# Kernel optimization log

Measured on AMD Instinct MI355X. Metric: run time of the kernel, lower is better.

Reference implementation:

```python
import jax, jax.numpy as jnp
from jax import lax
import numpy as np

B, T, C_IN, H, W = 2, 4, 128, 64, 64
D_MODEL, N_Q, N_POINTS, PATCH, N_LAYERS = 256, 300, 8, 3, 6


def _sine_pos(Hh, Ww, d, temperature=10000.0):
    # mask is all-False, so cumsum of ones -> arange(1..H)/H * 2pi
    two_pi = 2.0 * np.pi
    yn = (jnp.arange(1, Hh + 1, dtype=jnp.float32) / (Hh + 1e-6)) * two_pi
    xn = (jnp.arange(1, Ww + 1, dtype=jnp.float32) / (Ww + 1e-6)) * two_pi
    q = d // 4
    i = jnp.arange(q, dtype=jnp.float32)
    dim_t = temperature ** (2.0 * jnp.floor(i / 2.0) / q)
    py = yn[:, None] / dim_t
    px = xn[:, None] / dim_t
    py = jnp.stack([jnp.sin(py), jnp.cos(py)], axis=-1).reshape(Hh, 2 * q)
    px = jnp.stack([jnp.sin(px), jnp.cos(px)], axis=-1).reshape(Ww, 2 * q)
    pos = jnp.concatenate([
        jnp.broadcast_to(py[:, None, :], (Hh, Ww, 2 * q)),
        jnp.broadcast_to(px[None, :, :], (Hh, Ww, 2 * q)),
    ], axis=-1)
    return jnp.transpose(pos, (2, 0, 1))  # [d,H,W]


def _sample_scale(fmap, ref, ps):
    # fmap [B,C,h,w]; ref [B,nQ,nP,2] in [0,1]. Bilinear grid_sample,
    # padding_mode='border', align_corners=True -> direct gather (no replication).
    Bc, C, h, w = fmap.shape
    half = (ps - 1) / 2.0
    off = jnp.linspace(-half, half, ps, dtype=jnp.float32)
    oy, ox = jnp.meshgrid(off, off, indexing='ij')  # [ps,ps]
    gx = ref[..., 0, None, None] * 2.0 - 1.0 + ox * (2.0 / w)  # [B,nQ,nP,ps,ps]
    gy = ref[..., 1, None, None] * 2.0 - 1.0 + oy * (2.0 / h)
    x = jnp.clip((gx + 1.0) * 0.5 * (w - 1), 0.0, w - 1.0)
    y = jnp.clip((gy + 1.0) * 0.5 * (h - 1), 0.0, h - 1.0)
    x0 = jnp.floor(x); y0 = jnp.floor(y)
    wx = x - x0; wy = y - y0
    x0i = x0.astype(jnp.int32); y0i = y0.astype(jnp.int32)
    x1i = jnp.minimum(x0i + 1, w - 1); y1i = jnp.minimum(y0i + 1, h - 1)

    def per_b(fb, y0b, x0b, y1b, x1b, wxb, wyb):
        v00 = fb[:, y0b, x0b]  # [C,nQ,nP,ps,ps]
        v01 = fb[:, y0b, x1b]
        v10 = fb[:, y1b, x0b]
        v11 = fb[:, y1b, x1b]
        return (v00 * (1 - wxb) * (1 - wyb) + v01 * wxb * (1 - wyb)
                + v10 * (1 - wxb) * wyb + v11 * wxb * wyb)

    out = jax.vmap(per_b)(fmap, y0i, x0i, y1i, x1i, wx, wy)  # [B,C,nQ,nP,ps,ps]
    return jnp.transpose(out, (0, 2, 3, 4, 5, 1))  # [B,nQ,nP,ps,ps,C]


def reference(feat, pred_boxes_init, w_tf, b_tf, w_in, b_in, w_lat, b_lat, w_sm, b_sm,
              q_embed, q_pos, Wq, bq, Wo, bo, Wp1, bp1, Wp2, bp2,
              w_r1, b_r1, w_r2, b_r2, w_b1, b_b1, w_b2, b_b2, w_cls, b_cls):
    Bb, Tt, Cin, Hh, Ww = feat.shape
    d = w_in.shape[0]
    nP = w_r2.shape[0] // 2
    ps = int(round((Wp1.shape[-1] // d) ** 0.5))
    # temporal fuse: Conv3d kernel (3,1,1), padding (1,0,0)
    x = lax.conv_general_dilated(jnp.transpose(feat, (0, 2, 1, 3, 4)), w_tf,
                                 (1, 1, 1), [(1, 1), (0, 0), (0, 0)],
                                 dimension_numbers=('NCDHW', 'OIDHW', 'NCDHW'))
    x = x + b_tf[None, :, None, None, None]
    x = x.mean(axis=2)  # [B,Cin,H,W]
    x = jnp.einsum('bchw,dc->bdhw', x, w_in) + b_in[None, :, None, None]
    x = x + _sine_pos(Hh, Ww, d)[None]
    # FPN over scales {1,2,4}: avg_pool -> 1x1 lateral -> 3x3 smooth
    feats = []
    for i, s in enumerate((1, 2, 4)):
        xi = x if s == 1 else x.reshape(Bb, d, Hh // s, s, Ww // s, s).mean(axis=(3, 5))
        xi = jnp.einsum('bchw,oc->bohw', xi, w_lat[i]) + b_lat[i][None, :, None, None]
        xi = lax.conv_general_dilated(xi, w_sm[i], (1, 1), [(1, 1), (1, 1)],
                                      dimension_numbers=('NCHW', 'OIHW', 'NCHW'))
        xi = xi + b_sm[i][None, :, None, None]
        feats.append(xi)
    nQ = q_embed.shape[0]
    queries = jnp.broadcast_to((q_embed + q_pos)[None], (Bb, nQ, d))
    boxes = pred_boxes_init
    inv_sqrt_d = 1.0 / float(np.sqrt(d))
    for l in range(Wq.shape[0]):
        h1 = jax.nn.relu(jnp.einsum('bqd,od->bqo', queries, w_r1) + b_r1)
        ro = jnp.tanh(jnp.einsum('bqd,od->bqo', h1, w_r2) + b_r2)
        ro = ro.reshape(Bb, nQ, nP, 2) * 0.5
        ref = jnp.clip(boxes[:, :, None, :2] + ro, 0.0, 1.0)
        sampled = jnp.concatenate([_sample_scale(f, ref, ps) for f in feats], axis=2)
        sampled = sampled[:, :, :nP]  # truncate multi-scale concat back to nP
        flat = sampled.reshape(Bb, nQ, nP, ps * ps * d)
        pv = jax.nn.relu(jnp.einsum('bqpi,oi->bqpo', flat, Wp1[l]) + bp1[l])
        pv = jnp.einsum('bqpd,od->bqpo', pv, Wp2[l]) + bp2[l]
        kv = pv.mean(axis=2)  # [B,nP_q,d] -> [B,nQ,d]
        q = jnp.einsum('bqd,od->bqo', queries, Wq[l]) + bq[l]
        attn = jax.nn.softmax(jnp.einsum('bqd,bkd->bqk', q, kv) * inv_sqrt_d, axis=-1)
        out = jnp.einsum('bqk,bkd->bqd', attn, kv)
        queries = queries + (jnp.einsum('bqd,od->bqo', out, Wo[l]) + bo[l])
        hb = jax.nn.relu(jnp.einsum('bqd,od->bqo', queries, w_b1) + b_b1)
        delta = jax.nn.sigmoid(jnp.einsum('bqd,od->bqo', hb, w_b2) + b_b2)
        boxes = jnp.clip(boxes + 0.1 * jnp.tanh(delta - 0.5), 0.0, 1.0)
    logits = (jnp.einsum('bqd,od->bqo', queries, w_cls) + b_cls)[..., 0]
    return logits, boxes


def setup_inputs() -> dict:
    key = jax.random.key(0)
    keys = iter(jax.random.split(key, 48))

    def nrm(shape, s=0.02):
        return jax.random.normal(next(keys), shape, dtype=jnp.float32) * s

    inp = {
        'feat': jax.random.normal(next(keys), (B, T, C_IN, H, W), dtype=jnp.float32),
        'pred_boxes_init': jax.random.uniform(next(keys), (B, N_Q, 4), dtype=jnp.float32),
        'w_tf': nrm((C_IN, C_IN, 3, 1, 1)), 'b_tf': jnp.zeros((C_IN,), jnp.float32),
        'w_in': nrm((D_MODEL, C_IN)), 'b_in': jnp.zeros((D_MODEL,), jnp.float32),
        'w_lat': nrm((3, D_MODEL, D_MODEL)), 'b_lat': jnp.zeros((3, D_MODEL), jnp.float32),
        'w_sm': nrm((3, D_MODEL, D_MODEL, 3, 3)), 'b_sm': jnp.zeros((3, D_MODEL), jnp.float32),
        'q_embed': nrm((N_Q, D_MODEL), 1.0), 'q_pos': nrm((N_Q, D_MODEL), 1.0),
        'Wq': nrm((N_LAYERS, D_MODEL, D_MODEL)), 'bq': jnp.zeros((N_LAYERS, D_MODEL), jnp.float32),
        'Wo': nrm((N_LAYERS, D_MODEL, D_MODEL)), 'bo': jnp.zeros((N_LAYERS, D_MODEL), jnp.float32),
        'Wp1': nrm((N_LAYERS, D_MODEL, PATCH * PATCH * D_MODEL)), 'bp1': jnp.zeros((N_LAYERS, D_MODEL), jnp.float32),
        'Wp2': nrm((N_LAYERS, D_MODEL, D_MODEL)), 'bp2': jnp.zeros((N_LAYERS, D_MODEL), jnp.float32),
        'w_r1': nrm((D_MODEL, D_MODEL)), 'b_r1': jnp.zeros((D_MODEL,), jnp.float32),
        'w_r2': nrm((2 * N_POINTS, D_MODEL)), 'b_r2': jnp.zeros((2 * N_POINTS,), jnp.float32),
        'w_b1': nrm((D_MODEL, D_MODEL)), 'b_b1': jnp.zeros((D_MODEL,), jnp.float32),
        'w_b2': nrm((4, D_MODEL)), 'b_b2': jnp.zeros((4,), jnp.float32),
        'w_cls': nrm((1, D_MODEL)), 'b_cls': jnp.zeros((1,), jnp.float32),
    }
    return inp
```

## Files before the change

### kernel.cpp

```cpp
#include <hip/hip_runtime.h>
#include <hip/hip_bf16.h>
#include <math.h>

#define BB 2
#define TT 4
#define CIN 128
#define DM 256
#define NQ 300
#define NP 8
#define PS 3
#define NL 6
#define HW 4096
#define KP 2304

typedef __attribute__((ext_vector_type(8))) short short8;
typedef __attribute__((ext_vector_type(4))) short short4_t;
typedef __attribute__((ext_vector_type(4))) float f32x4;
typedef unsigned short ushort_t;

static __device__ __forceinline__ ushort_t f2bf(float f) {
  __hip_bfloat16 h = __float2bfloat16(f);
  return *reinterpret_cast<ushort_t*>(&h);
}
static __device__ __forceinline__ float bf2f(ushort_t u) {
  return __uint_as_float(((unsigned)u) << 16);
}

__global__ void k_prep(const float* __restrict__ w_in, const float* __restrict__ w_lat,
                       const float* __restrict__ w_b1,
                       const float* __restrict__ w_r1, const float* __restrict__ Wp1,
                       ushort_t* __restrict__ win_bf, ushort_t* __restrict__ wlat_bf,
                       ushort_t* __restrict__ wb1_bf,
                       ushort_t* __restrict__ wr1_bf, ushort_t* __restrict__ wp1_bf,
                       const float* __restrict__ w_tf, ushort_t* __restrict__ tct,
                       const float* __restrict__ w_sm, ushort_t* __restrict__ wsm_bf,
                       const float* __restrict__ Wp2, const float* __restrict__ Wo,
                       const float* __restrict__ bq, const float* __restrict__ bp2,
                       const float* __restrict__ bo,
                       float* __restrict__ bqt, float* __restrict__ bfuse,
                       uint4* __restrict__ x2p_zero,
                       const float* __restrict__ b_tf, const float* __restrict__ b_in,
                       float* __restrict__ bias_comb,
                       const float* __restrict__ qe, const float* __restrict__ qp,
                       const float* __restrict__ pb, float* __restrict__ queries,
                       ushort_t* __restrict__ qbf, float* __restrict__ boxes,
                       const float* __restrict__ feat, ushort_t* __restrict__ featT) {
  __shared__ float ldsF[64][65];
  float* bt = &ldsF[0][0];
  int b = blockIdx.x, t = threadIdx.x;
  if (b < 3680) {
    int i = b * 256 + t;
    const float* s; ushort_t* d; int base;
    if (i < 8192)         { s = w_in;  d = win_bf;  base = 0; }
    else if (i < 24576)   { s = w_lat; d = wlat_bf; base = 8192; }
    else if (i < 40960)   { s = w_b1;  d = wb1_bf;  base = 24576; }
    else if (i < 57344)   { s = w_r1;  d = wr1_bf;  base = 40960; }
    else                  { s = Wp1;   d = wp1_bf;  base = 57344; }
    int j = i - base;
    float4 v = ((const float4*)s)[j];
    d[j * 4 + 0] = f2bf(v.x);
    d[j * 4 + 1] = f2bf(v.y);
    d[j * 4 + 2] = f2bf(v.z);
    d[j * 4 + 3] = f2bf(v.w);
  } else if (b < 3936) {
    int i = (b - 3680) * 256 + t;
    int k = i >> 7, c = i & 127;
    int u = k >> 7, ci = k & 127;
    const float* wp = w_tf + ((size_t)(c * 128 + ci)) * 3;
    float w0 = wp[0], w1 = wp[1], w2 = wp[2];
    float coef = (u == 0) ? (w0 + w1) : (u == 3) ? (w1 + w2) : (w0 + w1 + w2);
    tct[(size_t)k * 128 + c] = f2bf(0.25f * coef);
  } else if (b < 6240) {
    int i = (b - 3936) * 256 + t;
    int n = i / KP;
    int r = i - n * KP;
    int tp = r >> 8, c = r & 255;
    wsm_bf[i] = f2bf(w_sm[((size_t)(n * 256 + c)) * 9 + tp]);
  } else if (b < 6252) {
    int i = (b - 6240) * 256 + t;
    if (i < 1536) {
      int l = i >> 8, d = i & 255;
      float a = 0.f;
      for (int o = 0; o < 256; ++o)
        a += bq[l * 256 + o] * Wp2[((size_t)(l * 256 + o)) * 256 + d];
      bqt[i] = a;
    } else {
      int j = i - 1536;
      int l = j >> 8, o2 = j & 255;
      float a = bo[l * 256 + o2];
      for (int o = 0; o < 256; ++o)
        a += bp2[l * 256 + o] * Wo[((size_t)(l * 256 + o2)) * 256 + o];
      bfuse[j] = a;
    }
  } else if (b < 7341) {
    int j = (b - 6252) * 256 + t;
    if (j < 278784) x2p_zero[j] = make_uint4(0u, 0u, 0u, 0u);
  } else if (b < 7342) {
    int d = t;
    if (d < 128) bt[d] = b_tf[d];
    __syncthreads();
    float a = b_in[d];
    for (int c = 0; c < 128; ++c) a += w_in[d * 128 + c] * bt[c];
    bias_comb[d] = a;
  } else if (b < 7942) {
    int i = (b - 7342) * 256 + t;
    if (i < BB * NQ * DM) {
      int rd = i % (NQ * DM);
      float v = qe[rd] + qp[rd];
      queries[i] = v;
      qbf[i] = f2bf(v);
    }
    if (i < BB * NQ * 4) boxes[i] = pb[i];
  } else {
    int idx = b - 7942;
    int gs = idx & 127;
    int k0 = (idx >> 7) * 64;
    int bb = gs >> 6;
    int s0 = (gs & 63) * 64;
    int kk = t >> 2, sc0 = (t & 3) * 16;
    {
      int k = k0 + kk;
      int u = k >> 7, ci = k & 127;
      const float* src = feat + (((size_t)(bb * 4 + u) * 128 + ci) << 12) + s0 + sc0;
#pragma unroll
      for (int j = 0; j < 4; ++j) {
        float4 v = *(const float4*)(src + j * 4);
        ldsF[kk][sc0 + j * 4 + 0] = v.x;
        ldsF[kk][sc0 + j * 4 + 1] = v.y;
        ldsF[kk][sc0 + j * 4 + 2] = v.z;
        ldsF[kk][sc0 + j * 4 + 3] = v.w;
      }
    }
    __syncthreads();
#pragma unroll
    for (int p = 0; p < 2; ++p) {
      int idx2 = p * 256 + t;
      int s_l = idx2 >> 3, kc = (idx2 & 7) * 8;
      short8 v;
#pragma unroll
      for (int j = 0; j < 8; ++j) v[j] = (short)f2bf(ldsF[kc + j][s_l]);
      *(short8*)(featT + (size_t)(bb * 4096 + s0 + s_l) * 512 + k0 + kc) = v;
    }
  }
}

__global__ __launch_bounds__(256) void k_wcompose(const float* __restrict__ Wp2,
                                                  const float* __restrict__ Wq,
                                                  const float* __restrict__ Wo,
                                                  ushort_t* __restrict__ wqt,
                                                  ushort_t* __restrict__ wfuseT) {
  __shared__ ushort_t As[64 * 36];
  __shared__ ushort_t Bs[64 * 36];
  int z = blockIdx.z, l = z % 6;
  const float* Asrc = Wp2 + (size_t)l * 65536;
  const float* Bsrc = ((z < 6) ? Wq : Wo) + (size_t)l * 65536;
  ushort_t* C = ((z < 6) ? wqt : wfuseT) + (size_t)l * 65536;
  bool btr = (z < 6);
  int tid = threadIdx.x;
  int bm = blockIdx.x * 64, bn = blockIdx.y * 64;
  int w = tid >> 6, lane = tid & 63;
  int wm = (w & 1) * 32, wn = (w >> 1) * 32;
  int q = lane >> 4, ml = lane & 15;
  f32x4 acc[2][2] = {};
  int oo = tid >> 3, mg = (tid & 7) * 8;
  int nr = tid >> 2, kg = (tid & 3) * 8;
  for (int k0 = 0; k0 < 256; k0 += 32) {
    {
      const float* sp = Asrc + (size_t)(k0 + oo) * 256 + bm + mg;
      float4 f0 = *(const float4*)sp;
      float4 f1 = *(const float4*)(sp + 4);
      ushort_t* dst = As + oo;
      dst[(mg + 0) * 36] = f2bf(f0.x); dst[(mg + 1) * 36] = f2bf(f0.y);
      dst[(mg + 2) * 36] = f2bf(f0.z); dst[(mg + 3) * 36] = f2bf(f0.w);
      dst[(mg + 4) * 36] = f2bf(f1.x); dst[(mg + 5) * 36] = f2bf(f1.y);
      dst[(mg + 6) * 36] = f2bf(f1.z); dst[(mg + 7) * 36] = f2bf(f1.w);
    }
    if (btr) {
      const float* sp = Bsrc + (size_t)(k0 + oo) * 256 + bn + mg;
      float4 f0 = *(const float4*)sp;
      float4 f1 = *(const float4*)(sp + 4);
      ushort_t* dst = Bs + oo;
      dst[(mg + 0) * 36] = f2bf(f0.x); dst[(mg + 1) * 36] = f2bf(f0.y);
      dst[(mg + 2) * 36] = f2bf(f0.z); dst[(mg + 3) * 36] = f2bf(f0.w);
      dst[(mg + 4) * 36] = f2bf(f1.x); dst[(mg + 5) * 36] = f2bf(f1.y);
      dst[(mg + 6) * 36] = f2bf(f1.z); dst[(mg + 7) * 36] = f2bf(f1.w);
    } else {
      const float* sp = Bsrc + (size_t)(bn + nr) * 256 + k0 + kg;
      float4 f0 = *(const float4*)sp;
      float4 f1 = *(const float4*)(sp + 4);
      short8 v;
      v[0] = (short)f2bf(f0.x); v[1] = (short)f2bf(f0.y);
      v[2] = (short)f2bf(f0.z); v[3] = (short)f2bf(f0.w);
      v[4] = (short)f2bf(f1.x); v[5] = (short)f2bf(f1.y);
      v[6] = (short)f2bf(f1.z); v[7] = (short)f2bf(f1.w);
      *(short8*)(Bs + nr * 36 + kg) = v;
    }
    __syncthreads();
    short8 a0 = *(const short8*)(As + (wm + ml) * 36 + q * 8);
    short8 a1 = *(const short8*)(As + (wm + 16 + ml) * 36 + q * 8);
    short8 b0 = *(const short8*)(Bs + (wn + ml) * 36 + q * 8);
    short8 b1 = *(const short8*)(Bs + (wn + 16 + ml) * 36 + q * 8);
    acc[0][0] = __builtin_amdgcn_mfma_f32_16x16x32_bf16(a0, b0, acc[0][0], 0, 0, 0);
    acc[0][1] = __builtin_amdgcn_mfma_f32_16x16x32_bf16(a0, b1, acc[0][1], 0, 0, 0);
    acc[1][0] = __builtin_amdgcn_mfma_f32_16x16x32_bf16(a1, b0, acc[1][0], 0, 0, 0);
    acc[1][1] = __builtin_amdgcn_mfma_f32_16x16x32_bf16(a1, b1, acc[1][1], 0, 0, 0);
    __syncthreads();
  }
#pragma unroll
  for (int i = 0; i < 2; ++i)
#pragma unroll
    for (int j = 0; j < 2; ++j) {
      int cn = bn + wn + j * 16 + ml;
#pragma unroll
      for (int r = 0; r < 4; ++r) {
        int rm = bm + wm + i * 16 + q * 4 + r;
        C[(size_t)rm * 256 + cn] = f2bf(acc[i][j][r]);
      }
    }
}

__global__ __launch_bounds__(256) void k_feat2(const ushort_t* __restrict__ featT,
                                               const ushort_t* __restrict__ wcomb,
                                               const float* __restrict__ biasc,
                                               ushort_t* __restrict__ xcl) {
  __shared__ ushort_t As[32 * 72];
  __shared__ ushort_t Bs[64 * 72];
  __shared__ float dimt_s[256];
  int tid = threadIdx.x;
  {
    int dd = tid & 127;
    int ii = dd >> 1;
    dimt_s[tid] = powf(10000.0f, (2.0f * (float)(ii >> 1)) / 64.0f);
  }
  int bm = blockIdx.x * 32, bn = blockIdx.y * 64;
  int w = tid >> 6, lane = tid & 63;
  int wm = (w & 1) * 16, wn = (w >> 1) * 32;
  int q = lane >> 4, ml = lane & 15;
  int sra = tid >> 3, sca = (tid & 7) * 8;
  int srb = tid >> 2, scb = (tid & 3) * 16;
  const ushort_t* Ag = featT + (size_t)(bm + sra) * 512 + sca;
  const ushort_t* Wg = wcomb + (size_t)(bn + srb) * 512 + scb;
  f32x4 acc[2] = {};
  short8 av = *(const short8*)Ag;
  short8 wv0 = *(const short8*)Wg;
  short8 wv1 = *(const short8*)(Wg + 8);
  for (int k0 = 0; k0 < 512; k0 += 64) {
    *(short8*)(As + sra * 72 + sca) = av;
    *(short8*)(Bs + srb * 72 + scb) = wv0;
    *(short8*)(Bs + srb * 72 + scb + 8) = wv1;
    __syncthreads();
    if (k0 + 64 < 512) {
      av = *(const short8*)(Ag + k0 + 64);
      wv0 = *(const short8*)(Wg + k0 + 64);
      wv1 = *(const short8*)(Wg + k0 + 72);
    }
#pragma unroll
    for (int h = 0; h < 2; ++h) {
      int kc = h * 32 + q * 8;
      short8 a = *(const short8*)(As + (wm + ml) * 72 + kc);
      short8 b0 = *(const short8*)(Bs + (wn + ml) * 72 + kc);
      short8 b1 = *(const short8*)(Bs + (wn + 16 + ml) * 72 + kc);
      acc[0] = __builtin_amdgcn_mfma_f32_16x16x32_bf16(a, b0, acc[0], 0, 0, 0);
      acc[1] = __builtin_amdgcn_mfma_f32_16x16x32_bf16(a, b1, acc[1], 0, 0, 0);
    }
    __syncthreads();
  }
  const float FKT = 6.28318530717958647692f / 64.000001f;
#pragma unroll
  for (int j = 0; j < 2; ++j) {
    int cn = bn + wn + j * 16 + ml;
    float dimt = dimt_s[cn];
    float bC = biasc[cn];
    bool isx = cn >= 128;
    bool isc = cn & 1;
#pragma unroll
    for (int r = 0; r < 4; ++r) {
      int rm = bm + wm + q * 4 + r;
      int s = rm & 4095;
      int y = s >> 6, x = s & 63;
      float ang = (float)((isx ? x : y) + 1) * FKT / dimt;
      float pos = isc ? cosf(ang) : sinf(ang);
      xcl[(size_t)rm * 256 + cn] = f2bf(acc[j][r] + bC + pos);
    }
  }
}

template <int ACT, int OUTMODE, int MG>
__global__ __launch_bounds__(256) void k_gemm_bf16(const ushort_t* __restrict__ A,
                                                   const ushort_t* __restrict__ W,
                                                   const float* __restrict__ bias,
                                                   const float* __restrict__ res,
                                                   float* __restrict__ Cf,
                                                   ushort_t* __restrict__ Cb,
                                                   int M, int N, int K,
                                                   const ushort_t* __restrict__ W2,
                                                   const float* __restrict__ bias2,
                                                   const ushort_t* __restrict__ W3,
                                                   const float* __restrict__ bias3) {
  __shared__ ushort_t As[64 * 72];
  __shared__ ushort_t Bs[64 * 72];
  int tid = threadIdx.x;
  int bm = blockIdx.x * 64, bn = blockIdx.y * 64;
  int w = tid >> 6, lane = tid & 63;
  int wm = (w & 1) * 32, wn = (w >> 1) * 32;
  int q = lane >> 4, ml = lane & 15;
  f32x4 acc[2][2] = {};
  int srow = tid >> 2, scol = (tid & 3) * 16;
  int ga = bm + srow;
  if (MG) ga = min(ga, M - 1);
  const ushort_t* Ag = A + (size_t)ga * K + scol;
  const ushort_t* Wg;
  if (OUTMODE == 7) {
    int seg = bn >> 8;
    const ushort_t* Wb = (seg == 0) ? W : ((seg == 1) ? W2 : W3);
    Wg = Wb + (size_t)((bn & 255) + srow) * K + scol;
  } else if (OUTMODE == 4) {
    const ushort_t* Wb = (bn < 256) ? W : W2;
    Wg = Wb + (size_t)((bn & 255) + srow) * K + scol;
  } else {
    Wg = W + (size_t)(bn + srow) * K + scol;
  }
  short8 av0 = *(const short8*)(Ag);
  short8 av1 = *(const short8*)(Ag + 8);
  short8 wv0 = *(const short8*)(Wg);
  short8 wv1 = *(const short8*)(Wg + 8);
  for (int k0 = 0; k0 < K; k0 += 64) {
    *(short8*)(As + srow * 72 + scol) = av0;
    *(short8*)(As + srow * 72 + scol + 8) = av1;
    *(short8*)(Bs + srow * 72 + scol) = wv0;
    *(short8*)(Bs + srow * 72 + scol + 8) = wv1;
    __syncthreads();
    if (k0 + 64 < K) {
      av0 = *(const short8*)(Ag + k0 + 64);
      av1 = *(const short8*)(Ag + k0 + 72);
      wv0 = *(const short8*)(Wg + k0 + 64);
      wv1 = *(const short8*)(Wg + k0 + 72);
    }
#pragma unroll
    for (int h = 0; h < 2; ++h) {
      int kc = h * 32 + q * 8;
      short8 a0 = *(const short8*)(As + (wm + ml) * 72 + kc);
      short8 a1 = *(const short8*)(As + (wm + 16 + ml) * 72 + kc);
      short8 b0 = *(const short8*)(Bs + (wn + ml) * 72 + kc);
      short8 b1 = *(const short8*)(Bs + (wn + 16 + ml) * 72 + kc);
      acc[0][0] = __builtin_amdgcn_mfma_f32_16x16x32_bf16(a0, b0, acc[0][0], 0, 0, 0);
      acc[0][1] = __builtin_amdgcn_mfma_f32_16x16x32_bf16(a0, b1, acc[0][1], 0, 0, 0);
      acc[1][0] = __builtin_amdgcn_mfma_f32_16x16x32_bf16(a1, b0, acc[1][0], 0, 0, 0);
      acc[1][1] = __builtin_amdgcn_mfma_f32_16x16x32_bf16(a1, b1, acc[1][1], 0, 0, 0);
    }
    __syncthreads();
  }
#pragma unroll
  for (int i = 0; i < 2; ++i) {
#pragma unroll
    for (int j = 0; j < 2; ++j) {
      int cn = bn + wn + j * 16 + ml;
      float bsv;
      if (OUTMODE == 7) {
        int seg = cn >> 8;
        bsv = ((seg == 0) ? bias : ((seg == 1) ? bias2 : bias3))[cn & 255];
      } else if (OUTMODE == 4) {
        bsv = ((cn < 256) ? bias : bias2)[cn & 255];
      } else {
        bsv = bias ? bias[cn] : 0.f;
      }
#pragma unroll
      for (int r = 0; r < 4; ++r) {
        int rm = bm + wm + i * 16 + q * 4 + r;
        if (MG && rm >= M) continue;
        float v = acc[i][j][r] + bsv;
        if (OUTMODE == 0) {
          if (ACT == 1) v = fmaxf(v, 0.f);
          Cf[(size_t)rm * N + cn] = v;
        } else if (OUTMODE == 1) {
          int b = rm >> 12, rem = rm & 4095;
          int y = rem >> 6, xx = rem & 63;
          Cb[(((size_t)(b * 66 + y + 1)) * 66 + xx + 1) * 256 + cn] = f2bf(v);
        } else if (OUTMODE == 4) {
          if (cn < 256) Cf[(size_t)rm * 256 + cn] = fmaxf(v, 0.f);
          else Cb[(size_t)rm * 256 + (cn & 255)] = f2bf(v);
        } else if (OUTMODE == 6) {
          Cb[(size_t)rm * N + cn] = f2bf(v);
        } else if (OUTMODE == 7) {
          if (cn < 256) Cf[(size_t)rm * 256 + cn] = fmaxf(v, 0.f);
          else if (cn < 512) ((float*)Cb)[(size_t)rm * 256 + (cn & 255)] = fmaxf(v, 0.f);
          else ((ushort_t*)res)[(size_t)rm * 256 + (cn & 255)] = f2bf(v);
        }
      }
    }
  }
}

__global__ __launch_bounds__(256) void k_wp1_split(const ushort_t* __restrict__ A,
                                                   const ushort_t* __restrict__ W,
                                                   ushort_t* __restrict__ part) {
  __shared__ ushort_t As[64 * 72];
  __shared__ ushort_t Bs[64 * 72];
  int tid = threadIdx.x;
  int bm = blockIdx.x * 64, bn = blockIdx.y * 64;
  int kz = blockIdx.z * 768;
  int w = tid >> 6, lane = tid & 63;
  int wm = (w & 1) * 32, wn = (w >> 1) * 32;
  int q = lane >> 4, ml = lane & 15;
  int srow = tid >> 2, scol = (tid & 3) * 16;
  const ushort_t* Ag = A + (size_t)(bm + srow) * KP + kz + scol;
  const ushort_t* Wg = W + (size_t)(bn + srow) * KP + kz + scol;
  f32x4 acc[2][2] = {};
  short8 av0 = *(const short8*)(Ag);
  short8 av1 = *(const short8*)(Ag + 8);
  short8 wv0 = *(const short8*)(Wg);
  short8 wv1 = *(const short8*)(Wg + 8);
  for (int k0 = 0; k0 < 768; k0 += 64) {
    *(short8*)(As + srow * 72 + scol) = av0;
    *(short8*)(As + srow * 72 + scol + 8) = av1;
    *(short8*)(Bs + srow * 72 + scol) = wv0;
    *(short8*)(Bs + srow * 72 + scol + 8) = wv1;
    __syncthreads();
    if (k0 + 64 < 768) {
      av0 = *(const short8*)(Ag + k0 + 64);
      av1 = *(const short8*)(Ag + k0 + 72);
      wv0 = *(const short8*)(Wg + k0 + 64);
      wv1 = *(const short8*)(Wg + k0 + 72);
    }
#pragma unroll
    for (int h = 0; h < 2; ++h) {
      int kc = h * 32 + q * 8;
      short8 a0 = *(const short8*)(As + (wm + ml) * 72 + kc);
      short8 a1 = *(const short8*)(As + (wm + 16 + ml) * 72 + kc);
      short8 b0 = *(const short8*)(Bs + (wn + ml) * 72 + kc);
      short8 b1 = *(const short8*)(Bs + (wn + 16 + ml) * 72 + kc);
      acc[0][0] = __builtin_amdgcn_mfma_f32_16x16x32_bf16(a0, b0, acc[0][0], 0, 0, 0);
      acc[0][1] = __builtin_amdgcn_mfma_f32_16x16x32_bf16(a0, b1, acc[0][1], 0, 0, 0);
      acc[1][0] = __builtin_amdgcn_mfma_f32_16x16x32_bf16(a1, b0, acc[1][0], 0, 0, 0);
      acc[1][1] = __builtin_amdgcn_mfma_f32_16x16x32_bf16(a1, b1, acc[1][1], 0, 0, 0);
    }
    __syncthreads();
  }
  ushort_t* pz = part + (size_t)blockIdx.z * 4800 * 256;
#pragma unroll
  for (int i = 0; i < 2; ++i)
#pragma unroll
    for (int j = 0; j < 2; ++j) {
      int cn = bn + wn + j * 16 + ml;
#pragma unroll
      for (int r = 0; r < 4; ++r) {
        int rm = bm + wm + i * 16 + q * 4 + r;
        pz[(size_t)rm * 256 + cn] = f2bf(acc[i][j][r]);
      }
    }
}

__global__ __launch_bounds__(256) void k_wp1_reduce(const ushort_t* __restrict__ part,
                                                    const float* __restrict__ bias,
                                                    ushort_t* __restrict__ pvm) {
  int row = blockIdx.x;
  int d = threadIdx.x;
  float b = bias[d];
  float s = 0.f;
#pragma unroll
  for (int p = 0; p < 8; ++p) {
    size_t idx = (size_t)(row * 8 + p) * 256 + d;
    float v = bf2f(part[idx]) + bf2f(part[idx + (size_t)4800 * 256]) +
              bf2f(part[idx + (size_t)2 * 4800 * 256]) + b;
    s += fmaxf(v, 0.f);
  }
  pvm[(size_t)row * 256 + d] = f2bf(s * 0.125f);
}

__global__ __launch_bounds__(256) void k_conv3(const ushort_t* __restrict__ x2p,
                                               const ushort_t* __restrict__ wsm,
                                               const float* __restrict__ bsm,
                                               ushort_t* __restrict__ fcl) {
  __shared__ ushort_t As[32 * 72];
  __shared__ ushort_t Bs[64 * 72];
  int tid = threadIdx.x;
  int bm = blockIdx.x * 32, bn = blockIdx.y * 64;
  int w = tid >> 6, lane = tid & 63;
  int wm = (w & 1) * 16, wn = (w >> 1) * 32;
  int q = lane >> 4, ml = lane & 15;
  int sra = tid >> 3, sca = (tid & 7) * 8;
  int srb = tid >> 2, scb = (tid & 3) * 16;
  int sA = bm + sra;
  int b = sA >> 12, rem = sA & 4095;
  size_t pbase = ((size_t)(b * 66 + (rem >> 6)) * 66 + (rem & 63)) * 256;
  const ushort_t* Wg = wsm + (size_t)(bn + srb) * KP + scb;
  auto loadA = [&](int k0) {
    int ka = k0 + sca;
    int t9 = ka >> 8;
    int ky = t9 / 3, kx = t9 - ky * 3;
    return *(const short8*)(x2p + pbase + (size_t)(ky * 66 + kx) * 256 + (ka & 255));
  };
  f32x4 acc[2] = {};
  short8 av = loadA(0);
  short8 wv0 = *(const short8*)(Wg);
  short8 wv1 = *(const short8*)(Wg + 8);
  for (int k0 = 0; k0 < KP; k0 += 64) {
    *(short8*)(As + sra * 72 + sca) = av;
    *(short8*)(Bs + srb * 72 + scb) = wv0;
    *(short8*)(Bs + srb * 72 + scb + 8) = wv1;
    __syncthreads();
    if (k0 + 64 < KP) {
      av = loadA(k0 + 64);
      wv0 = *(const short8*)(Wg + k0 + 64);
      wv1 = *(const short8*)(Wg + k0 + 72);
    }
#pragma unroll
    for (int h = 0; h < 2; ++h) {
      int kc = h * 32 + q * 8;
      short8 a = *(const short8*)(As + (wm + ml) * 72 + kc);
      short8 b0 = *(const short8*)(Bs + (wn + ml) * 72 + kc);
      short8 b1 = *(const short8*)(Bs + (wn + 16 + ml) * 72 + kc);
      acc[0] = __builtin_amdgcn_mfma_f32_16x16x32_bf16(a, b0, acc[0], 0, 0, 0);
      acc[1] = __builtin_amdgcn_mfma_f32_16x16x32_bf16(a, b1, acc[1], 0, 0, 0);
    }
    __syncthreads();
  }
#pragma unroll
  for (int j = 0; j < 2; ++j) {
    int cn = bn + wn + j * 16 + ml;
    float bsv = bsm[cn];
#pragma unroll
    for (int r = 0; r < 4; ++r) {
      int rm = bm + wm + q * 4 + r;
      fcl[(size_t)rm * 256 + cn] = f2bf(acc[j][r] + bsv);
    }
  }
}

__global__ __launch_bounds__(256) void k_sample(const ushort_t* __restrict__ fcl,
                                                const float* __restrict__ h1,
                                                const float* __restrict__ w_r2,
                                                const float* __restrict__ b_r2,
                                                const float* __restrict__ boxesIn,
                                                float* __restrict__ boxesOut,
                                                const float* __restrict__ hb,
                                                const float* __restrict__ w_b2,
                                                const float* __restrict__ b_b2,
                                                ushort_t* __restrict__ flat) {
  __shared__ float pr[8];
  __shared__ float bc2[2];
  __shared__ float nb2[2];
  int blk = blockIdx.x;
  int row = blk >> 3, p = blk & 7;
  int b = row / NQ;
  int tid = threadIdx.x;
  int w = tid >> 6, lane = tid & 63;
  if (hb) {
    float4 hv = *(const float4*)(hb + (size_t)row * 256 + lane * 4);
    float4 wv = *(const float4*)(w_b2 + (size_t)w * 256 + lane * 4);
    float aa = hv.x * wv.x + hv.y * wv.y + hv.z * wv.z + hv.w * wv.w;
#pragma unroll
    for (int s = 32; s > 0; s >>= 1) aa += __shfl_down(aa, s, 64);
    if (lane == 0) {
      aa += b_b2[w];
      float delta = 1.0f / (1.0f + expf(-aa));
      float v = boxesIn[row * 4 + w] + 0.1f * tanhf(delta - 0.5f);
      v = fminf(fmaxf(v, 0.f), 1.f);
      if (w < 2) nb2[w] = v;
      if (p == 0) boxesOut[row * 4 + w] = v;
    }
  } else if (tid < 2) {
    nb2[tid] = boxesIn[row * 4 + tid];
  }
  float h = h1[(size_t)row * 256 + tid];
  float px = h * w_r2[(size_t)(2 * p) * 256 + tid];
  float py = h * w_r2[(size_t)(2 * p + 1) * 256 + tid];
#pragma unroll
  for (int s = 32; s > 0; s >>= 1) {
    px += __shfl_down(px, s, 64);
    py += __shfl_down(py, s, 64);
  }
  if (lane == 0) { pr[w * 2] = px; pr[w * 2 + 1] = py; }
  __syncthreads();
  if (tid == 0) {
    float sx = pr[0] + pr[2] + pr[4] + pr[6] + b_r2[2 * p];
    float sy = pr[1] + pr[3] + pr[5] + pr[7] + b_r2[2 * p + 1];
    float rx = nb2[0] + 0.5f * tanhf(sx);
    float ry = nb2[1] + 0.5f * tanhf(sy);
    bc2[0] = fminf(fmaxf(rx, 0.f), 1.f);
    bc2[1] = fminf(fmaxf(ry, 0.f), 1.f);
  }
  __syncthreads();
  float rx = bc2[0], ry = bc2[1];
  const ushort_t* fb = fcl + (size_t)b * HW * DM;
  ushort_t* op = flat + (size_t)blk * KP;
  int c4 = (tid & 63) * 4;
  int g = tid >> 6;
  int p0 = (g == 0) ? 0 : (1 + 2 * g);
  int p1 = (g == 0) ? 3 : (3 + 2 * g);
  for (int p9 = p0; p9 < p1; ++p9) {
    int jy = (p9 >= 6) ? 2 : ((p9 >= 3) ? 1 : 0);
    int jx = p9 - jy * 3;
    float yy = (ry + (float)(jy - 1) * (1.0f / 64.0f)) * 63.0f;
    yy = fminf(fmaxf(yy, 0.f), 63.0f);
    float y0f = floorf(yy);
    float wy = yy - y0f;
    int y0 = (int)y0f;
    int y1 = min(y0 + 1, 63);
    float xx = (rx + (float)(jx - 1) * (1.0f / 64.0f)) * 63.0f;
    xx = fminf(fmaxf(xx, 0.f), 63.0f);
    float x0f = floorf(xx);
    float wx = xx - x0f;
    int x0 = (int)x0f;
    int x1 = min(x0 + 1, 63);
    short4_t v00 = *(const short4_t*)(fb + (y0 * 64 + x0) * DM + c4);
    short4_t v01 = *(const short4_t*)(fb + (y0 * 64 + x1) * DM + c4);
    short4_t v10 = *(const short4_t*)(fb + (y1 * 64 + x0) * DM + c4);
    short4_t v11 = *(const short4_t*)(fb + (y1 * 64 + x1) * DM + c4);
    short4_t ov;
#pragma unroll
    for (int jj = 0; jj < 4; ++jj) {
      float v = bf2f((ushort_t)v00[jj]) * (1.f - wx) * (1.f - wy) +
                bf2f((ushort_t)v01[jj]) * wx * (1.f - wy) +
                bf2f((ushort_t)v10[jj]) * (1.f - wx) * wy +
                bf2f((ushort_t)v11[jj]) * wx * wy;
      ov[jj] = (short)f2bf(v);
    }
    *(short4_t*)(op + p9 * DM + c4) = ov;
  }
}

__global__ __launch_bounds__(256) void k_attn(const ushort_t* __restrict__ qt,
                                              const ushort_t* __restrict__ pvm,
                                              const ushort_t* __restrict__ wfT,
                                              const float* __restrict__ bfuse_l,
                                              float* __restrict__ queries,
                                              ushort_t* __restrict__ qbf) {
  __shared__ float qs[256];
  __shared__ float sc[512];
  __shared__ float red[256];
  __shared__ float pr4[1024];
  int row = blockIdx.x;
  int b = row / NQ;
  int tid = threadIdx.x;
  qs[tid] = bf2f(qt[(size_t)row * DM + tid]);
  __syncthreads();
  const ushort_t* kvB = pvm + (size_t)b * NQ * DM;
#pragma unroll
  for (int s2 = 0; s2 < 2; ++s2) {
    int k = tid + s2 * 256;
    float v = -1e30f;
    if (k < NQ) {
      const ushort_t* kp = kvB + (size_t)k * DM;
      float a = 0.f;
#pragma unroll
      for (int d = 0; d < 256; d += 8) {
        short8 k8 = *(const short8*)(kp + d);
        const float* qd = qs + d;
        a += bf2f((ushort_t)k8[0]) * qd[0];
        a += bf2f((ushort_t)k8[1]) * qd[1];
        a += bf2f((ushort_t)k8[2]) * qd[2];
        a += bf2f((ushort_t)k8[3]) * qd[3];
        a += bf2f((ushort_t)k8[4]) * qd[4];
        a += bf2f((ushort_t)k8[5]) * qd[5];
        a += bf2f((ushort_t)k8[6]) * qd[6];
        a += bf2f((ushort_t)k8[7]) * qd[7];
      }
      v = a * (1.0f / 16.0f);
    }
    sc[k] = v;
  }
  __syncthreads();
  red[tid] = fmaxf(sc[tid], sc[tid + 256]);
  __syncthreads();
  for (int st = 128; st > 0; st >>= 1) {
    if (tid < st) red[tid] = fmaxf(red[tid], red[tid + st]);
    __syncthreads();
  }
  float mx = red[0];
  __syncthreads();
  float e0 = (tid < NQ) ? expf(sc[tid] - mx) : 0.f;
  float e1 = (tid + 256 < NQ) ? expf(sc[tid + 256] - mx) : 0.f;
  sc[tid] = e0;
  sc[tid + 256] = e1;
  red[tid] = e0 + e1;
  __syncthreads();
  for (int st = 128; st > 0; st >>= 1) {
    if (tid < st) red[tid] += red[tid + st];
    __syncthreads();
  }
  float inv = 1.0f / red[0];
  __syncthreads();
  float acc = 0.f;
#pragma unroll 4
  for (int k = 0; k < NQ; ++k)
    acc += sc[k] * bf2f(kvB[(size_t)k * DM + tid]);
  qs[tid] = acc * inv;
  __syncthreads();
  int oq = (tid & 63) * 4, dq = (tid >> 6) * 64;
  float a0 = 0.f, a1 = 0.f, a2 = 0.f, a3 = 0.f;
  const ushort_t* wp = wfT + (size_t)dq * 256 + oq;
#pragma unroll 8
  for (int dd = 0; dd < 64; ++dd) {
    float cc = qs[dq + dd];
    short4_t wv = *(const short4_t*)(wp + (size_t)dd * 256);
    a0 += cc * bf2f((ushort_t)wv[0]);
    a1 += cc * bf2f((ushort_t)wv[1]);
    a2 += cc * bf2f((ushort_t)wv[2]);
    a3 += cc * bf2f((ushort_t)wv[3]);
  }
  float* pb4 = pr4 + (tid >> 6) * 256 + oq;
  pb4[0] = a0; pb4[1] = a1; pb4[2] = a2; pb4[3] = a3;
  __syncthreads();
  float v = pr4[tid] + pr4[256 + tid] + pr4[512 + tid] + pr4[768 + tid] +
            bfuse_l[tid] + queries[(size_t)row * DM + tid];
  queries[(size_t)row * DM + tid] = v;
  qbf[(size_t)row * DM + tid] = f2bf(v);
}

__global__ __launch_bounds__(256) void k_boxf(const float* __restrict__ hb,
                                              const float* __restrict__ w_b2,
                                              const float* __restrict__ b_b2,
                                              float* __restrict__ boxes,
                                              int last,
                                              const float* __restrict__ queries,
                                              const float* __restrict__ w_cls,
                                              const float* __restrict__ b_cls,
                                              float* __restrict__ out) {
  __shared__ float nb[4];
  int row = blockIdx.x;
  int tid = threadIdx.x;
  int j = tid >> 6, lane = tid & 63;
  float4 hv = *(const float4*)(hb + (size_t)row * 256 + lane * 4);
  float4 wv = *(const float4*)(w_b2 + (size_t)j * 256 + lane * 4);
  float aa = hv.x * wv.x + hv.y * wv.y + hv.z * wv.z + hv.w * wv.w;
#pragma unroll
  for (int s = 32; s > 0; s >>= 1) aa += __shfl_down(aa, s, 64);
  if (lane == 0) {
    aa += b_b2[j];
    float delta = 1.0f / (1.0f + expf(-aa));
    float v = boxes[row * 4 + j] + 0.1f * tanhf(delta - 0.5f);
    v = fminf(fmaxf(v, 0.f), 1.f);
    boxes[row * 4 + j] = v;
    nb[j] = v;
  }
  if (last) {
    __syncthreads();
    if (j == 0) {
      float4 qv = *(const float4*)(queries + (size_t)row * 256 + lane * 4);
      float4 cv = *(const float4*)(w_cls + lane * 4);
      float a2 = qv.x * cv.x + qv.y * cv.y + qv.z * cv.z + qv.w * cv.w;
#pragma unroll
      for (int s = 32; s > 0; s >>= 1) a2 += __shfl_down(a2, s, 64);
      if (lane == 0) out[row] = a2 + b_cls[0];
    } else if (j == 1 && lane < 4) {
      out[600 + row * 4 + lane] = nb[lane];
    }
  }
}

extern "C" void kernel_launch(void* const* d_in, const int* in_sizes, int n_in,
                              void* d_out, int out_size, void* d_ws, size_t ws_size,
                              hipStream_t stream) {
  const float* feat   = (const float*)d_in[0];
  const float* pb     = (const float*)d_in[1];
  const float* w_tf   = (const float*)d_in[2];
  const float* b_tf   = (const float*)d_in[3];
  const float* w_in   = (const float*)d_in[4];
  const float* b_in   = (const float*)d_in[5];
  const float* w_lat  = (const float*)d_in[6];
  const float* b_lat  = (const float*)d_in[7];
  const float* w_sm   = (const float*)d_in[8];
  const float* b_sm   = (const float*)d_in[9];
  const float* q_embed= (const float*)d_in[10];
  const float* q_pos  = (const float*)d_in[11];
  const float* Wq     = (const float*)d_in[12];
  const float* bq     = (const float*)d_in[13];
  const float* Wo     = (const float*)d_in[14];
  const float* bo     = (const float*)d_in[15];
  const float* Wp1    = (const float*)d_in[16];
  const float* bp1    = (const float*)d_in[17];
  const float* Wp2    = (const float*)d_in[18];
  const float* bp2    = (const float*)d_in[19];
  const float* w_r1   = (const float*)d_in[20];
  const float* b_r1   = (const float*)d_in[21];
  const float* w_r2   = (const float*)d_in[22];
  const float* b_r2   = (const float*)d_in[23];
  const float* w_b1   = (const float*)d_in[24];
  const float* b_b1   = (const float*)d_in[25];
  const float* w_b2   = (const float*)d_in[26];
  const float* b_b2   = (const float*)d_in[27];
  const float* w_cls  = (const float*)d_in[28];
  const float* b_cls  = (const float*)d_in[29];
  float* out = (float*)d_out;

  float* ws = (float*)d_ws;
  size_t off = 0;
  auto alloc = [&](size_t n) { float* p = ws + off; off += n; return p; };
  ushort_t* flat    = (ushort_t*)alloc(5529600);
  ushort_t* part    = (ushort_t*)alloc(1843200);
  ushort_t* featT   = (ushort_t*)alloc(2097152);
  ushort_t* xcl     = (ushort_t*)alloc(1048576);
  ushort_t* x2p     = (ushort_t*)alloc(1115136);
  ushort_t* fcl     = (ushort_t*)alloc(1048576);
  ushort_t* wcomb   = (ushort_t*)alloc(65536);
  ushort_t* tct     = (ushort_t*)alloc(32768);
  ushort_t* win_bf  = (ushort_t*)alloc(16384);
  float*    biasc   = alloc(256);
  ushort_t* wlat_bf = (ushort_t*)alloc(32768);
  ushort_t* wsm_bf  = (ushort_t*)alloc(294912);
  ushort_t* wp1_bf  = (ushort_t*)alloc(1769472);
  ushort_t* wb1_bf  = (ushort_t*)alloc(32768);
  ushort_t* wr1_bf  = (ushort_t*)alloc(32768);
  ushort_t* wqt_bf  = (ushort_t*)alloc(196608);
  ushort_t* wfuseT  = (ushort_t*)alloc(196608);
  float*    bqt     = alloc(1536);
  float*    bfuse   = alloc(1536);
  float* queries = alloc(153600);
  ushort_t* qbf  = (ushort_t*)alloc(76800);
  float* h1      = alloc(153600);
  ushort_t* qt   = (ushort_t*)alloc(76800);
  float* hb      = alloc(153600);
  ushort_t* pvm  = (ushort_t*)alloc(76800);
  float* boxesA  = alloc(2400);
  float* boxesB  = alloc(2400);
  (void)ws_size; (void)in_sizes; (void)n_in; (void)out_size;

  k_prep<<<8966, 256, 0, stream>>>(w_in, w_lat, w_b1, w_r1, Wp1,
                                   win_bf, wlat_bf, wb1_bf, wr1_bf, wp1_bf,
                                   w_tf, tct, w_sm, wsm_bf,
                                   Wp2, Wo, bq, bp2, bo, bqt, bfuse,
                                   (uint4*)x2p, b_tf, b_in, biasc,
                                   q_embed, q_pos, pb, queries, qbf, boxesA,
                                   feat, featT);
  k_gemm_bf16<0, 6, 0><<<dim3(4, 8), 256, 0, stream>>>(win_bf, tct, nullptr, nullptr,
                                                       nullptr, wcomb, 256, 512, 128,
                                                       nullptr, nullptr, nullptr, nullptr);
  k_wcompose<<<dim3(4, 4, 12), 256, 0, stream>>>(Wp2, Wq, Wo, wqt_bf, wfuseT);

  k_feat2<<<dim3(256, 4), 256, 0, stream>>>(featT, wcomb, biasc, xcl);
  k_gemm_bf16<0, 1, 0><<<dim3(128, 4), 256, 0, stream>>>(xcl, wlat_bf, b_lat, nullptr,
                                                         nullptr, x2p, BB * HW, 256, 256,
                                                         nullptr, nullptr, nullptr, nullptr);
  k_conv3<<<dim3(256, 4), 256, 0, stream>>>(x2p, wsm_bf, b_sm, fcl);

  const int M6 = BB * NQ;
  const int Mp = BB * NQ * NP;
  dim3 g600w((M6 + 63) / 64, 8);
  dim3 g600m((M6 + 63) / 64, 12);
  dim3 gsk(Mp / 64, 4, 3);

  k_gemm_bf16<0, 4, 1><<<g600w, 256, 0, stream>>>(qbf, wr1_bf, b_r1, nullptr, h1,
                                                  qt, M6, 512, 256,
                                                  wqt_bf, bqt, nullptr, nullptr);
  float* bcur = boxesA;
  float* bnext = boxesB;
  for (int l = 0; l < NL; ++l) {
    const float* hbp = (l == 0) ? nullptr : hb;
    k_sample<<<Mp, 256, 0, stream>>>(fcl, h1, w_r2, b_r2, bcur, bnext,
                                     hbp, w_b2, b_b2, flat);
    if (l > 0) { float* tmp = bcur; bcur = bnext; bnext = tmp; }
    k_wp1_split<<<gsk, 256, 0, stream>>>(flat, wp1_bf + (size_t)l * 256 * KP, part);
    k_wp1_reduce<<<600, 256, 0, stream>>>(part, bp1 + (size_t)l * DM, pvm);
    k_attn<<<M6, 256, 0, stream>>>(qt, pvm, wfuseT + (size_t)l * 65536,
                                   bfuse + l * 256, queries, qbf);
    int ln = (l + 1) % NL;
    k_gemm_bf16<0, 7, 1><<<g600m, 256, 0, stream>>>(qbf, wb1_bf, b_b1, (const float*)qt,
                                                    hb, (ushort_t*)h1, M6, 768, 256,
                                                    wr1_bf, b_r1,
                                                    wqt_bf + (size_t)ln * 65536,
                                                    bqt + ln * 256);
  }
  k_boxf<<<M6, 256, 0, stream>>>(hb, w_b2, b_b2, bcur, 1,
                                 queries, w_cls, b_cls, out);
}
```

Measured before the change: 669.0 us.

## Fuse Wp1 split-K GEMM and reduce into one kernel with epilogue pooling

Replaces the 3-way split-K Wp1 GEMM, which wrote bf16 partials, and its separate reduce kernel with a single full-K GEMM. It uses 32-row M tiles and applies bias, ReLU and the mean over the 8 points in the epilogue through a lane shuffle. This removes the partial-buffer round trip and one launch per layer. In exchange each block now runs a longer K loop, with 600 blocks instead of 900, and the partials are no longer rounded to bf16 before summing.

```diff
diff --git a/kernel.cpp b/kernel.cpp
--- a/kernel.cpp
+++ b/kernel.cpp
@@ -391,80 +391,59 @@
   }
 }
 
-__global__ __launch_bounds__(256) void k_wp1_split(const ushort_t* __restrict__ A,
-                                                   const ushort_t* __restrict__ W,
-                                                   ushort_t* __restrict__ part) {
-  __shared__ ushort_t As[64 * 72];
+__global__ __launch_bounds__(256) void k_wp1(const ushort_t* __restrict__ A,
+                                             const ushort_t* __restrict__ W,
+                                             const float* __restrict__ bias,
+                                             ushort_t* __restrict__ pvm) {
+  __shared__ ushort_t As[32 * 72];
   __shared__ ushort_t Bs[64 * 72];
   int tid = threadIdx.x;
-  int bm = blockIdx.x * 64, bn = blockIdx.y * 64;
-  int kz = blockIdx.z * 768;
+  int bm = blockIdx.x * 32, bn = blockIdx.y * 64;
   int w = tid >> 6, lane = tid & 63;
-  int wm = (w & 1) * 32, wn = (w >> 1) * 32;
+  int wm = (w & 1) * 16, wn = (w >> 1) * 32;
   int q = lane >> 4, ml = lane & 15;
-  int srow = tid >> 2, scol = (tid & 3) * 16;
-  const ushort_t* Ag = A + (size_t)(bm + srow) * KP + kz + scol;
-  const ushort_t* Wg = W + (size_t)(bn + srow) * KP + kz + scol;
-  f32x4 acc[2][2] = {};
-  short8 av0 = *(const short8*)(Ag);
-  short8 av1 = *(const short8*)(Ag + 8);
+  int sra = tid >> 3, sca = (tid & 7) * 8;
+  int srb = tid >> 2, scb = (tid & 3) * 16;
+  const ushort_t* Ag = A + (size_t)(bm + sra) * KP + sca;
+  const ushort_t* Wg = W + (size_t)(bn + srb) * KP + scb;
+  f32x4 acc[2] = {};
+  short8 av = *(const short8*)(Ag);
   short8 wv0 = *(const short8*)(Wg);
   short8 wv1 = *(const short8*)(Wg + 8);
-  for (int k0 = 0; k0 < 768; k0 += 64) {
-    *(short8*)(As + srow * 72 + scol) = av0;
-    *(short8*)(As + srow * 72 + scol + 8) = av1;
-    *(short8*)(Bs + srow * 72 + scol) = wv0;
-    *(short8*)(Bs + srow * 72 + scol + 8) = wv1;
-    __syncthreads();
-    if (k0 + 64 < 768) {
-      av0 = *(const short8*)(Ag + k0 + 64);
-      av1 = *(const short8*)(Ag + k0 + 72);
+  for (int k0 = 0; k0 < KP; k0 += 64) {
+    *(short8*)(As + sra * 72 + sca) = av;
+    *(short8*)(Bs + srb * 72 + scb) = wv0;
+    *(short8*)(Bs + srb * 72 + scb + 8) = wv1;
+    __syncthreads();
+    if (k0 + 64 < KP) {
+      av = *(const short8*)(Ag + k0 + 64);
       wv0 = *(const short8*)(Wg + k0 + 64);
       wv1 = *(const short8*)(Wg + k0 + 72);
     }
 #pragma unroll
     for (int h = 0; h < 2; ++h) {
       int kc = h * 32 + q * 8;
-      short8 a0 = *(const short8*)(As + (wm + ml) * 72 + kc);
-      short8 a1 = *(const short8*)(As + (wm + 16 + ml) * 72 + kc);
+      short8 a = *(const short8*)(As + (wm + ml) * 72 + kc);
       short8 b0 = *(const short8*)(Bs + (wn + ml) * 72 + kc);
       short8 b1 = *(const short8*)(Bs + (wn + 16 + ml) * 72 + kc);
-      acc[0][0] = __builtin_amdgcn_mfma_f32_16x16x32_bf16(a0, b0, acc[0][0], 0, 0, 0);
-      acc[0][1] = __builtin_amdgcn_mfma_f32_16x16x32_bf16(a0, b1, acc[0][1], 0, 0, 0);
-      acc[1][0] = __builtin_amdgcn_mfma_f32_16x16x32_bf16(a1, b0, acc[1][0], 0, 0, 0);
-      acc[1][1] = __builtin_amdgcn_mfma_f32_16x16x32_bf16(a1, b1, acc[1][1], 0, 0, 0);
-    }
-    __syncthreads();
-  }
-  ushort_t* pz = part + (size_t)blockIdx.z * 4800 * 256;
-#pragma unroll
-  for (int i = 0; i < 2; ++i)
-#pragma unroll
-    for (int j = 0; j < 2; ++j) {
-      int cn = bn + wn + j * 16 + ml;
-#pragma unroll
-      for (int r = 0; r < 4; ++r) {
-        int rm = bm + wm + i * 16 + q * 4 + r;
-        pz[(size_t)rm * 256 + cn] = f2bf(acc[i][j][r]);
-      }
-    }
-}
-
-__global__ __launch_bounds__(256) void k_wp1_reduce(const ushort_t* __restrict__ part,
-                                                    const float* __restrict__ bias,
-                                                    ushort_t* __restrict__ pvm) {
-  int row = blockIdx.x;
-  int d = threadIdx.x;
-  float b = bias[d];
-  float s = 0.f;
-#pragma unroll
-  for (int p = 0; p < 8; ++p) {
-    size_t idx = (size_t)(row * 8 + p) * 256 + d;
-    float v = bf2f(part[idx]) + bf2f(part[idx + (size_t)4800 * 256]) +
-              bf2f(part[idx + (size_t)2 * 4800 * 256]) + b;
-    s += fmaxf(v, 0.f);
-  }
-  pvm[(size_t)row * 256 + d] = f2bf(s * 0.125f);
+      acc[0] = __builtin_amdgcn_mfma_f32_16x16x32_bf16(a, b0, acc[0], 0, 0, 0);
+      acc[1] = __builtin_amdgcn_mfma_f32_16x16x32_bf16(a, b1, acc[1], 0, 0, 0);
+    }
+    __syncthreads();
+  }
+#pragma unroll
+  for (int j = 0; j < 2; ++j) {
+    int cn = bn + wn + j * 16 + ml;
+    float bsv = bias[cn];
+    float s = 0.f;
+#pragma unroll
+    for (int r = 0; r < 4; ++r) s += fmaxf(acc[j][r] + bsv, 0.f);
+    s += __shfl_xor(s, 16, 64);
+    if ((q & 1) == 0) {
+      int prow = ((bm + wm) >> 3) + (q >> 1);
+      pvm[(size_t)prow * 256 + cn] = f2bf(s * 0.125f);
+    }
+  }
 }
 
 __global__ __launch_bounds__(256) void k_conv3(const ushort_t* __restrict__ x2p,
@@ -788,7 +767,6 @@
   size_t off = 0;
   auto alloc = [&](size_t n) { float* p = ws + off; off += n; return p; };
   ushort_t* flat    = (ushort_t*)alloc(5529600);
-  ushort_t* part    = (ushort_t*)alloc(1843200);
   ushort_t* featT   = (ushort_t*)alloc(2097152);
   ushort_t* xcl     = (ushort_t*)alloc(1048576);
   ushort_t* x2p     = (ushort_t*)alloc(1115136);
@@ -838,7 +816,7 @@
   const int Mp = BB * NQ * NP;
   dim3 g600w((M6 + 63) / 64, 8);
   dim3 g600m((M6 + 63) / 64, 12);
-  dim3 gsk(Mp / 64, 4, 3);
+  dim3 gw1(Mp / 32, 4);
 
   k_gemm_bf16<0, 4, 1><<<g600w, 256, 0, stream>>>(qbf, wr1_bf, b_r1, nullptr, h1,
                                                   qt, M6, 512, 256,
@@ -850,8 +828,8 @@
     k_sample<<<Mp, 256, 0, stream>>>(fcl, h1, w_r2, b_r2, bcur, bnext,
                                      hbp, w_b2, b_b2, flat);
     if (l > 0) { float* tmp = bcur; bcur = bnext; bnext = tmp; }
-    k_wp1_split<<<gsk, 256, 0, stream>>>(flat, wp1_bf + (size_t)l * 256 * KP, part);
-    k_wp1_reduce<<<600, 256, 0, stream>>>(part, bp1 + (size_t)l * DM, pvm);
+    k_wp1<<<gw1, 256, 0, stream>>>(flat, wp1_bf + (size_t)l * 256 * KP,
+                                   bp1 + (size_t)l * DM, pvm);
     k_attn<<<M6, 256, 0, stream>>>(qt, pvm, wfuseT + (size_t)l * 65536,
                                    bfuse + l * 256, queries, qbf);
     int ln = (l + 1) % NL;
```

After: 674.1 us. No clear change (+0.8%).
